# Kernel optimization log

Measured on AMD Instinct MI355X. Metric: run time of the kernel, lower is better.

## Reference

```python
import jax, jax.numpy as jnp
import numpy as np
import math

B, T, C, H, DFF = 4, 2048, 1024, 16, 4096
HD = C // H
EPS = 1e-5


def _layernorm(x, g, b):
    mu = jnp.mean(x, axis=-1, keepdims=True)
    var = jnp.var(x, axis=-1, keepdims=True)
    return (x - mu) * jax.lax.rsqrt(var + EPS) * g + b


def _new_gelu(x):
    # 0.5*x*(1+tanh(sqrt(2/pi)*(x+0.044715*x^3)))
    c = math.sqrt(2.0 / math.pi)
    return 0.5 * x * (1.0 + jnp.tanh(c * (x + 0.044715 * x ** 3)))


def setup_inputs() -> dict:
    key = jax.random.key(0)
    ks = jax.random.split(key, 12)
    s = lambda fan_in: 1.0 / math.sqrt(fan_in)
    return {
        "x": jax.random.normal(ks[0], (B, T, C), jnp.float32),
        "ln1_g": jnp.ones((C,), jnp.float32),
        "ln1_b": jnp.zeros((C,), jnp.float32),
        "w_qkv": jax.random.normal(ks[1], (C, 3 * C), jnp.float32) * s(C),
        "b_qkv": jnp.zeros((3 * C,), jnp.float32),
        "w_o": jax.random.normal(ks[2], (C, C), jnp.float32) * s(C),
        "b_o": jnp.zeros((C,), jnp.float32),
        "ln2_g": jnp.ones((C,), jnp.float32),
        "ln2_b": jnp.zeros((C,), jnp.float32),
        "w_fc": jax.random.normal(ks[3], (C, DFF), jnp.float32) * s(C),
        "b_fc": jnp.zeros((DFF,), jnp.float32),
        "w_proj": jax.random.normal(ks[4], (DFF, C), jnp.float32) * s(DFF),
        "b_proj": jnp.zeros((C,), jnp.float32),
    }


def reference(x, ln1_g, ln1_b, w_qkv, b_qkv, w_o, b_o, ln2_g, ln2_b, w_fc, b_fc, w_proj, b_proj):
    # --- attention sub-block ---
    h = _layernorm(x, ln1_g, ln1_b)
    qkv = h @ w_qkv + b_qkv                                  # (B,T,3C)
    q, k, v = jnp.split(qkv, 3, axis=-1)
    q = q.reshape(B, T, H, HD).transpose(0, 2, 1, 3)          # (B,H,T,hd)
    k = k.reshape(B, T, H, HD).transpose(0, 2, 1, 3)
    v = v.reshape(B, T, H, HD).transpose(0, 2, 1, 3)
    scores = jnp.einsum("bhqd,bhkd->bhqk", q, k) / math.sqrt(HD)
    causal = jnp.tril(jnp.ones((T, T), jnp.bool_))            # (T,T)
    scores = jnp.where(causal[None, None], scores, -jnp.inf)
    probs = jax.nn.softmax(scores, axis=-1)
    attn = jnp.einsum("bhqk,bhkd->bhqd", probs, v)
    attn = attn.transpose(0, 2, 1, 3).reshape(B, T, C)
    x = x + attn @ w_o + b_o
    # --- MLP sub-block ---
    h2 = _layernorm(x, ln2_g, ln2_b)
    x = x + _new_gelu(h2 @ w_fc + b_fc) @ w_proj + b_proj
    return x
```

## Files before the change

kernel.cpp:

```cpp
#include <hip/hip_runtime.h>
#include <hip/hip_bf16.h>

using bf16 = __hip_bfloat16;
typedef __attribute__((ext_vector_type(8))) short bf16x8;
typedef __attribute__((ext_vector_type(4))) float f32x4;
typedef __attribute__((ext_vector_type(16))) float f32x16;

#define LOG2E 1.4426950408889634f

__device__ inline short f2b(float f) {
  __hip_bfloat16 h = __float2bfloat16(f);
  return *reinterpret_cast<short*>(&h);
}
__device__ inline float b2f(short s) {
  unsigned int u = ((unsigned int)(unsigned short)s) << 16;
  float f;
  __builtin_memcpy(&f, &u, 4);
  return f;
}
__device__ inline unsigned pk2(float a, float b) {
  return (unsigned)(unsigned short)f2b(a) |
         ((unsigned)(unsigned short)f2b(b) << 16);
}

__global__ __launch_bounds__(256) void transpose_cast_kernel(
    const float* __restrict__ in, bf16* __restrict__ out, int K, int N) {
  __shared__ float tile[32][33];
  int tx = threadIdx.x & 31;
  int ty = threadIdx.x >> 5;
  int n0 = blockIdx.x * 32, k0 = blockIdx.y * 32;
#pragma unroll
  for (int i = 0; i < 4; i++)
    tile[ty + i * 8][tx] = in[(size_t)(k0 + ty + i * 8) * N + n0 + tx];
  __syncthreads();
#pragma unroll
  for (int i = 0; i < 4; i++)
    out[(size_t)(n0 + ty + i * 8) * K + k0 + tx] =
        __float2bfloat16(tile[tx][ty + i * 8]);
}

__global__ __launch_bounds__(256) void transpose_v_kernel(
    const bf16* __restrict__ qkv, bf16* __restrict__ vt) {
  __shared__ short tile[64][66];
  const int bh = blockIdx.y;
  const int b = bh >> 4, h = bh & 15;
  const int t0 = blockIdx.x * 64;
  const int tid = threadIdx.x;
  const int r = tid >> 3, c8 = (tid & 7) * 8;
#pragma unroll
  for (int p = 0; p < 2; p++) {
    int t = r + p * 32;
    bf16x8 v = *(const bf16x8*)&qkv[(size_t)(b * 2048 + t0 + t) * 3072 + 2048 +
                                    h * 64 + c8];
#pragma unroll
    for (int i = 0; i < 8; i++) tile[t][c8 + i] = v[i];
  }
  __syncthreads();
#pragma unroll
  for (int p = 0; p < 2; p++) {
    int d = r + p * 32;
    int tt = c8;
    bf16x8 o;
#pragma unroll
    for (int i = 0; i < 8; i++) o[i] = tile[tt + i][d];
    *(bf16x8*)&vt[(size_t)(bh * 64 + d) * 2048 + t0 + tt] = o;
  }
}

__global__ __launch_bounds__(256) void ln_kernel(
    const float* __restrict__ x, const float* __restrict__ g,
    const float* __restrict__ b, bf16* __restrict__ out) {
  int row = blockIdx.x;
  const float4 v = ((const float4*)(x + (size_t)row * 1024))[threadIdx.x];
  float s = v.x + v.y + v.z + v.w;
  float ss = v.x * v.x + v.y * v.y + v.z * v.z + v.w * v.w;
#pragma unroll
  for (int off = 1; off < 64; off <<= 1) {
    s += __shfl_xor(s, off);
    ss += __shfl_xor(ss, off);
  }
  __shared__ float red[2][4];
  int w = threadIdx.x >> 6, lane = threadIdx.x & 63;
  if (lane == 0) { red[0][w] = s; red[1][w] = ss; }
  __syncthreads();
  s = red[0][0] + red[0][1] + red[0][2] + red[0][3];
  ss = red[1][0] + red[1][1] + red[1][2] + red[1][3];
  float mu = s * (1.0f / 1024.0f);
  float var = ss * (1.0f / 1024.0f) - mu * mu;
  float rstd = rsqrtf(var + 1e-5f);
  const float4 gv = ((const float4*)g)[threadIdx.x];
  const float4 bv = ((const float4*)b)[threadIdx.x];
  short4 o4;
  o4.x = f2b((v.x - mu) * rstd * gv.x + bv.x);
  o4.y = f2b((v.y - mu) * rstd * gv.y + bv.y);
  o4.z = f2b((v.z - mu) * rstd * gv.z + bv.z);
  o4.w = f2b((v.w - mu) * rstd * gv.w + bv.w);
  ((short4*)out)[(size_t)row * 256 + threadIdx.x] = o4;
}

template <int EPI>
__global__ __launch_bounds__(256) void gemm_bt_kernel(
    const bf16* __restrict__ A, const bf16* __restrict__ Bt,
    const float* __restrict__ bias, const float* __restrict__ res,
    void* __restrict__ out, int M, int N, int K) {
  __shared__ short As[128 * 32];
  __shared__ short Bs[128 * 32];
  const int tid = threadIdx.x;
  const int w = tid >> 6, lane = tid & 63;
  const int wr = w >> 1, wc = w & 1;
  const int brow = blockIdx.y, bcol = blockIdx.x;

  f32x4 acc[4][4] = {};

  const int nk = K >> 5;
  for (int kt = 0; kt < nk; kt++) {
    __syncthreads();
#pragma unroll
    for (int j = 0; j < 2; j++) {
      int c = (j * 4 + w) * 64 + lane;
      int row = c >> 2, k8 = (c & 3) * 8;
      const bf16* ga = A + (size_t)(brow * 128 + row) * K + kt * 32 + k8;
      __builtin_amdgcn_global_load_lds(
          (const __attribute__((address_space(1))) unsigned int*)ga,
          (__attribute__((address_space(3))) unsigned int*)(As + (j * 4 + w) * 512),
          16, 0, 0);
      const bf16* gb = Bt + (size_t)(bcol * 128 + row) * K + kt * 32 + k8;
      __builtin_amdgcn_global_load_lds(
          (const __attribute__((address_space(1))) unsigned int*)gb,
          (__attribute__((address_space(3))) unsigned int*)(Bs + (j * 4 + w) * 512),
          16, 0, 0);
    }
    __syncthreads();
    bf16x8 af[4], bfr[4];
#pragma unroll
    for (int m = 0; m < 4; m++)
      af[m] = *(const bf16x8*)&As[(wr * 64 + m * 16 + (lane & 15)) * 32 +
                                  (lane >> 4) * 8];
#pragma unroll
    for (int n = 0; n < 4; n++)
      bfr[n] = *(const bf16x8*)&Bs[(wc * 64 + n * 16 + (lane & 15)) * 32 +
                                   (lane >> 4) * 8];
#pragma unroll
    for (int m = 0; m < 4; m++)
#pragma unroll
      for (int n = 0; n < 4; n++)
        acc[m][n] = __builtin_amdgcn_mfma_f32_16x16x32_bf16(af[m], bfr[n],
                                                            acc[m][n], 0, 0, 0);
  }

#pragma unroll
  for (int m = 0; m < 4; m++)
#pragma unroll
    for (int n = 0; n < 4; n++) {
      int gr0 = brow * 128 + wr * 64 + m * 16 + (lane >> 4) * 4;
      int gc = bcol * 128 + wc * 64 + n * 16 + (lane & 15);
      float bia = bias[gc];
#pragma unroll
      for (int j = 0; j < 4; j++) {
        float v = acc[m][n][j] + bia;
        size_t idx = (size_t)(gr0 + j) * N + gc;
        if constexpr (EPI == 0) {
          ((bf16*)out)[idx] = __float2bfloat16(v);
        } else if constexpr (EPI == 1) {
          ((float*)out)[idx] = v + res[idx];
        } else {
          float u = 0.7978845608028654f * (v + 0.044715f * v * v * v);
          float t = exp2f(u * (2.0f * LOG2E));
          float th = 1.0f - 2.0f / (t + 1.0f);
          ((bf16*)out)[idx] = __float2bfloat16(0.5f * v * (1.0f + th));
        }
      }
    }
}

__global__ __launch_bounds__(256) void attn_kernel(
    const bf16* __restrict__ qkv, const bf16* __restrict__ vt,
    bf16* __restrict__ attn) {
  const int bh = blockIdx.x;
  const int qt = blockIdx.y;
  const int b = bh >> 4, h = bh & 15;
  const int tid = threadIdx.x, w = tid >> 6, lane = tid & 63;
  const int col = lane & 31;
  const int hi = lane >> 5;

  __shared__ short Kl[64 * 64];
  __shared__ short Vl[64 * 64];

  const int qbase = qt * 128 + w * 32;
  const int qglob = qbase + col;
  const size_t qrow = (size_t)(b * 2048 + qglob);

  bf16x8 qf[4];
#pragma unroll
  for (int dks = 0; dks < 4; dks++) {
    bf16x8 raw =
        *(const bf16x8*)&qkv[qrow * 3072 + h * 64 + dks * 16 + hi * 8];
#pragma unroll
    for (int i = 0; i < 8; i++) qf[dks][i] = f2b(b2f(raw[i]) * 0.125f);
  }

  f32x16 ot[2] = {};
  float m = -1e30f, l = 0.0f;

  const int ktend = qt * 2 + 1;
  for (int kt = 0; kt <= ktend; kt++) {
    const int kv0 = kt * 64;
    __syncthreads();
#pragma unroll
    for (int j = 0; j < 2; j++) {
      int c = (j * 4 + w) * 64 + lane;
      int row = c >> 3;
      int sw8 = ((c & 7) ^ (row & 7)) * 8;
      const bf16* gk =
          qkv + (size_t)(b * 2048 + kv0 + row) * 3072 + 1024 + h * 64 + sw8;
      __builtin_amdgcn_global_load_lds(
          (const __attribute__((address_space(1))) unsigned int*)gk,
          (__attribute__((address_space(3))) unsigned int*)(Kl + (j * 4 + w) * 512),
          16, 0, 0);
      const bf16* gv = vt + (size_t)(bh * 64 + row) * 2048 + kv0 + sw8;
      __builtin_amdgcn_global_load_lds(
          (const __attribute__((address_space(1))) unsigned int*)gv,
          (__attribute__((address_space(3))) unsigned int*)(Vl + (j * 4 + w) * 512),
          16, 0, 0);
    }
    __syncthreads();

    if (kv0 <= qbase + 31) {
      f32x16 st[2] = {};
#pragma unroll
      for (int s = 0; s < 2; s++) {
        int kvrow = s * 32 + col;
        int swz = kvrow & 7;
#pragma unroll
        for (int dks = 0; dks < 4; dks++) {
          int ch = (dks * 2 + hi) ^ swz;
          bf16x8 kf = *(const bf16x8*)&Kl[kvrow * 64 + ch * 8];
          st[s] = __builtin_amdgcn_mfma_f32_32x32x16_bf16(kf, qf[dks], st[s],
                                                          0, 0, 0);
        }
      }
      if (kv0 + 63 > qbase) {
#pragma unroll
        for (int s = 0; s < 2; s++)
#pragma unroll
          for (int r = 0; r < 16; r++) {
            int kv = kv0 + s * 32 + (r & 3) + 8 * (r >> 2) + 4 * hi;
            if (kv > qglob) st[s][r] = -1e30f;
          }
      }
      float pmax = -1e30f;
#pragma unroll
      for (int s = 0; s < 2; s++)
#pragma unroll
        for (int r = 0; r < 16; r++) pmax = fmaxf(pmax, st[s][r]);
      pmax = fmaxf(pmax, __shfl_xor(pmax, 32));
      float mnew = fmaxf(m, pmax);
      float corr = exp2f((m - mnew) * LOG2E);
      m = mnew;
      float rs = 0.0f;
#pragma unroll
      for (int s = 0; s < 2; s++)
#pragma unroll
        for (int r = 0; r < 16; r++) {
          float pv = exp2f((st[s][r] - mnew) * LOG2E);
          st[s][r] = pv;
          rs += pv;
        }
      rs += __shfl_xor(rs, 32);
      l = l * corr + rs;
#pragma unroll
      for (int s = 0; s < 2; s++)
#pragma unroll
        for (int r = 0; r < 16; r++) ot[s][r] *= corr;

#pragma unroll
      for (int sub = 0; sub < 2; sub++) {
#pragma unroll
        for (int kl = 0; kl < 2; kl++) {
          unsigned A0 = pk2(st[sub][kl * 8 + 0], st[sub][kl * 8 + 1]);
          unsigned A1 = pk2(st[sub][kl * 8 + 2], st[sub][kl * 8 + 3]);
          unsigned B0 = pk2(st[sub][kl * 8 + 4], st[sub][kl * 8 + 5]);
          unsigned B1 = pk2(st[sub][kl * 8 + 6], st[sub][kl * 8 + 7]);
          unsigned sA0 = (unsigned)__shfl_xor((int)A0, 32);
          unsigned sA1 = (unsigned)__shfl_xor((int)A1, 32);
          unsigned sB0 = (unsigned)__shfl_xor((int)B0, 32);
          unsigned sB1 = (unsigned)__shfl_xor((int)B1, 32);
          union { unsigned u[4]; bf16x8 v; } pf;
          pf.u[0] = hi ? sB0 : A0;
          pf.u[1] = hi ? sB1 : A1;
          pf.u[2] = hi ? B0 : sA0;
          pf.u[3] = hi ? B1 : sA1;
          int ks = sub * 2 + kl;
#pragma unroll
          for (int ds = 0; ds < 2; ds++) {
            int drow = ds * 32 + col;
            int ch = (ks * 2 + hi) ^ (drow & 7);
            bf16x8 vf = *(const bf16x8*)&Vl[drow * 64 + ch * 8];
            ot[ds] = __builtin_amdgcn_mfma_f32_32x32x16_bf16(vf, pf.v, ot[ds],
                                                             0, 0, 0);
          }
        }
      }
    }
  }

  float rl = 1.0f / l;
#pragma unroll
  for (int ds = 0; ds < 2; ds++)
#pragma unroll
    for (int j = 0; j < 4; j++) {
      ushort4 o4;
      o4.x = (unsigned short)f2b(ot[ds][4 * j + 0] * rl);
      o4.y = (unsigned short)f2b(ot[ds][4 * j + 1] * rl);
      o4.z = (unsigned short)f2b(ot[ds][4 * j + 2] * rl);
      o4.w = (unsigned short)f2b(ot[ds][4 * j + 3] * rl);
      *(ushort4*)&attn[qrow * 1024 + h * 64 + 32 * ds + 8 * j + 4 * hi] = o4;
    }
}

extern "C" void kernel_launch(void* const* d_in, const int* in_sizes, int n_in,
                              void* d_out, int out_size, void* d_ws,
                              size_t ws_size, hipStream_t stream) {
  (void)in_sizes; (void)n_in; (void)out_size; (void)ws_size;
  const float* x      = (const float*)d_in[0];
  const float* ln1_g  = (const float*)d_in[1];
  const float* ln1_b  = (const float*)d_in[2];
  const float* w_qkv  = (const float*)d_in[3];
  const float* b_qkv  = (const float*)d_in[4];
  const float* w_o    = (const float*)d_in[5];
  const float* b_o    = (const float*)d_in[6];
  const float* ln2_g  = (const float*)d_in[7];
  const float* ln2_b  = (const float*)d_in[8];
  const float* w_fc   = (const float*)d_in[9];
  const float* b_fc   = (const float*)d_in[10];
  const float* w_proj = (const float*)d_in[11];
  const float* b_proj = (const float*)d_in[12];
  float* out = (float*)d_out;

  char* ws = (char*)d_ws;
  bf16* wt_qkv  = (bf16*)(ws + 0);
  bf16* wt_o    = (bf16*)(ws + 6291456);
  bf16* wt_fc   = (bf16*)(ws + 8388608);
  bf16* wt_proj = (bf16*)(ws + 16777216);
  float* x1     = (float*)(ws + 25165824);
  bf16* vtb     = (bf16*)(ws + 25165824);
  bf16* slotA   = (bf16*)(ws + 58720256);
  bf16* qkvb    = (bf16*)(ws + 75497472);
  bf16* gbuf    = (bf16*)(ws + 75497472);

  dim3 blk(256);
  transpose_cast_kernel<<<dim3(3072 / 32, 1024 / 32), blk, 0, stream>>>(
      w_qkv, wt_qkv, 1024, 3072);
  transpose_cast_kernel<<<dim3(1024 / 32, 1024 / 32), blk, 0, stream>>>(
      w_o, wt_o, 1024, 1024);
  transpose_cast_kernel<<<dim3(4096 / 32, 1024 / 32), blk, 0, stream>>>(
      w_fc, wt_fc, 1024, 4096);
  transpose_cast_kernel<<<dim3(1024 / 32, 4096 / 32), blk, 0, stream>>>(
      w_proj, wt_proj, 4096, 1024);

  ln_kernel<<<8192, blk, 0, stream>>>(x, ln1_g, ln1_b, slotA);
  gemm_bt_kernel<0><<<dim3(3072 / 128, 8192 / 128), blk, 0, stream>>>(
      slotA, wt_qkv, b_qkv, nullptr, qkvb, 8192, 3072, 1024);
  transpose_v_kernel<<<dim3(32, 64), blk, 0, stream>>>(qkvb, vtb);
  attn_kernel<<<dim3(64, 16), blk, 0, stream>>>(qkvb, vtb, slotA);
  gemm_bt_kernel<1><<<dim3(1024 / 128, 8192 / 128), blk, 0, stream>>>(
      slotA, wt_o, b_o, x, x1, 8192, 1024, 1024);
  ln_kernel<<<8192, blk, 0, stream>>>(x1, ln2_g, ln2_b, slotA);
  gemm_bt_kernel<2><<<dim3(4096 / 128, 8192 / 128), blk, 0, stream>>>(
      slotA, wt_fc, b_fc, nullptr, gbuf, 8192, 4096, 1024);
  gemm_bt_kernel<1><<<dim3(1024 / 128, 8192 / 128), blk, 0, stream>>>(
      gbuf, wt_proj, b_proj, x1, out, 8192, 1024, 4096);
}
```

Measured before the change: 471.3 us.

## Replace GEMM with 8-wave 128x256 double-buffered pipelined MFMA kernel

Measured after the change: 480.5 us. Within noise of the previous version (+2.0%).

```diff
diff --git a/kernel.cpp b/kernel.cpp
--- a/kernel.cpp
+++ b/kernel.cpp
@@ -98,54 +98,125 @@
   ((short4*)out)[(size_t)row * 256 + threadIdx.x] = o4;
 }
 
+template <int MLO, int NLO>
+__device__ inline void quad_mfma(f32x4 (&acc)[4][4], bf16x8 (&af)[2][2],
+                                 bf16x8 (&bf)[2][2]) {
+  __builtin_amdgcn_s_barrier();
+  asm volatile("s_waitcnt lgkmcnt(0)" ::: "memory");
+  __builtin_amdgcn_sched_barrier(0);
+  __builtin_amdgcn_s_setprio(1);
+#pragma unroll
+  for (int mm = 0; mm < 2; mm++)
+#pragma unroll
+    for (int nn = 0; nn < 2; nn++)
+#pragma unroll
+      for (int ks = 0; ks < 2; ks++)
+        acc[MLO + mm][NLO + nn] = __builtin_amdgcn_mfma_f32_16x16x32_bf16(
+            af[mm][ks], bf[nn][ks], acc[MLO + mm][NLO + nn], 0, 0, 0);
+  __builtin_amdgcn_s_setprio(0);
+  __builtin_amdgcn_s_barrier();
+}
+
 template <int EPI>
-__global__ __launch_bounds__(256) void gemm_bt_kernel(
+__global__ __launch_bounds__(512, 1) void gemm_bt8_kernel(
     const bf16* __restrict__ A, const bf16* __restrict__ Bt,
     const float* __restrict__ bias, const float* __restrict__ res,
     void* __restrict__ out, int M, int N, int K) {
-  __shared__ short As[128 * 32];
-  __shared__ short Bs[128 * 32];
+  __shared__ short As[2][128 * 64];
+  __shared__ short Bs[2][256 * 64];
   const int tid = threadIdx.x;
-  const int w = tid >> 6, lane = tid & 63;
-  const int wr = w >> 1, wc = w & 1;
-  const int brow = blockIdx.y, bcol = blockIdx.x;
+  const int lane = tid & 63, wid = tid >> 6;
+  const int wr = wid >> 2, wc = wid & 3;
+
+  const int nwg = gridDim.x;
+  const int gy = M >> 7;
+  const int flat = blockIdx.x;
+  const int sw = (flat & 7) * (nwg >> 3) + (flat >> 3);
+  const int bcol = sw / gy, brow = sw % gy;
+
+  const int nk = K >> 6;
+
+  auto stA = [&](int kt, int buf) {
+#pragma unroll
+    for (int r = 0; r < 2; r++) {
+      const int row = tid >> 3;
+      const int chs = (tid & 7) ^ (row & 7);
+      const bf16* src =
+          A + (size_t)(brow * 128 + r * 64 + row) * K + kt * 64 + chs * 8;
+      __builtin_amdgcn_global_load_lds(
+          (const __attribute__((address_space(1))) unsigned int*)src,
+          (__attribute__((address_space(3))) unsigned int*)
+              &As[buf][(r * 64 + wid * 8) * 64],
+          16, 0, 0);
+    }
+  };
+  auto stB = [&](int kt, int buf, int r0) {
+#pragma unroll
+    for (int rr = 0; rr < 2; rr++) {
+      const int r = r0 + rr;
+      const int row = tid >> 3;
+      const int chs = (tid & 7) ^ (row & 7);
+      const bf16* src =
+          Bt + (size_t)(bcol * 256 + r * 64 + row) * K + kt * 64 + chs * 8;
+      __builtin_amdgcn_global_load_lds(
+          (const __attribute__((address_space(1))) unsigned int*)src,
+          (__attribute__((address_space(3))) unsigned int*)
+              &Bs[buf][(r * 64 + wid * 8) * 64],
+          16, 0, 0);
+    }
+  };
 
   f32x4 acc[4][4] = {};
-
-  const int nk = K >> 5;
-  for (int kt = 0; kt < nk; kt++) {
-    __syncthreads();
-#pragma unroll
-    for (int j = 0; j < 2; j++) {
-      int c = (j * 4 + w) * 64 + lane;
-      int row = c >> 2, k8 = (c & 3) * 8;
-      const bf16* ga = A + (size_t)(brow * 128 + row) * K + kt * 32 + k8;
-      __builtin_amdgcn_global_load_lds(
-          (const __attribute__((address_space(1))) unsigned int*)ga,
-          (__attribute__((address_space(3))) unsigned int*)(As + (j * 4 + w) * 512),
-          16, 0, 0);
-      const bf16* gb = Bt + (size_t)(bcol * 128 + row) * K + kt * 32 + k8;
-      __builtin_amdgcn_global_load_lds(
-          (const __attribute__((address_space(1))) unsigned int*)gb,
-          (__attribute__((address_space(3))) unsigned int*)(Bs + (j * 4 + w) * 512),
-          16, 0, 0);
-    }
-    __syncthreads();
-    bf16x8 af[4], bfr[4];
-#pragma unroll
-    for (int m = 0; m < 4; m++)
-      af[m] = *(const bf16x8*)&As[(wr * 64 + m * 16 + (lane & 15)) * 32 +
-                                  (lane >> 4) * 8];
-#pragma unroll
-    for (int n = 0; n < 4; n++)
-      bfr[n] = *(const bf16x8*)&Bs[(wc * 64 + n * 16 + (lane & 15)) * 32 +
-                                   (lane >> 4) * 8];
-#pragma unroll
-    for (int m = 0; m < 4; m++)
-#pragma unroll
-      for (int n = 0; n < 4; n++)
-        acc[m][n] = __builtin_amdgcn_mfma_f32_16x16x32_bf16(af[m], bfr[n],
-                                                            acc[m][n], 0, 0, 0);
+  bf16x8 af[2][2], bf0[2][2], bf1[2][2];
+  int cur = 0;
+
+  auto rdA = [&](int mh) {
+#pragma unroll
+    for (int mm = 0; mm < 2; mm++)
+#pragma unroll
+      for (int ks = 0; ks < 2; ks++) {
+        const int row = wr * 64 + (mh * 2 + mm) * 16 + (lane & 15);
+        const int ch = (ks * 4 + (lane >> 4)) ^ (row & 7);
+        af[mm][ks] = *(const bf16x8*)&As[cur][row * 64 + ch * 8];
+      }
+  };
+  auto rdB = [&](bf16x8(&bf)[2][2], int nh) {
+#pragma unroll
+    for (int nn = 0; nn < 2; nn++)
+#pragma unroll
+      for (int ks = 0; ks < 2; ks++) {
+        const int row = wc * 64 + (nh * 2 + nn) * 16 + (lane & 15);
+        const int ch = (ks * 4 + (lane >> 4)) ^ (row & 7);
+        bf[nn][ks] = *(const bf16x8*)&Bs[cur][row * 64 + ch * 8];
+      }
+  };
+
+  stA(0, 0);
+  stB(0, 0, 0);
+  stB(0, 0, 2);
+  stA(1, 1);
+  asm volatile("s_waitcnt vmcnt(2)" ::: "memory");
+  __builtin_amdgcn_s_barrier();
+
+  for (int t = 0; t < nk; t++) {
+    cur = t & 1;
+    const int nxt = cur ^ 1;
+    rdA(0);
+    rdB(bf0, 0);
+    if (t + 1 < nk) stB(t + 1, nxt, 0);
+    quad_mfma<0, 0>(acc, af, bf0);
+    rdB(bf1, 1);
+    if (t + 1 < nk) stB(t + 1, nxt, 2);
+    quad_mfma<0, 2>(acc, af, bf1);
+    rdA(1);
+    quad_mfma<2, 2>(acc, af, bf1);
+    if (t + 2 < nk) {
+      stA(t + 2, cur);
+      asm volatile("s_waitcnt vmcnt(2)" ::: "memory");
+    } else if (t + 1 < nk) {
+      asm volatile("s_waitcnt vmcnt(0)" ::: "memory");
+    }
+    quad_mfma<2, 0>(acc, af, bf0);
   }
 
 #pragma unroll
@@ -153,7 +224,7 @@
 #pragma unroll
     for (int n = 0; n < 4; n++) {
       int gr0 = brow * 128 + wr * 64 + m * 16 + (lane >> 4) * 4;
-      int gc = bcol * 128 + wc * 64 + n * 16 + (lane & 15);
+      int gc = bcol * 256 + wc * 64 + n * 16 + (lane & 15);
       float bia = bias[gc];
 #pragma unroll
       for (int j = 0; j < 4; j++) {
@@ -165,8 +236,8 @@
           ((float*)out)[idx] = v + res[idx];
         } else {
           float u = 0.7978845608028654f * (v + 0.044715f * v * v * v);
-          float t = exp2f(u * (2.0f * LOG2E));
-          float th = 1.0f - 2.0f / (t + 1.0f);
+          float t2 = exp2f(u * (2.0f * LOG2E));
+          float th = 1.0f - 2.0f / (t2 + 1.0f);
           ((bf16*)out)[idx] = __float2bfloat16(0.5f * v * (1.0f + th));
         }
       }
@@ -359,15 +430,15 @@
       w_proj, wt_proj, 4096, 1024);
 
   ln_kernel<<<8192, blk, 0, stream>>>(x, ln1_g, ln1_b, slotA);
-  gemm_bt_kernel<0><<<dim3(3072 / 128, 8192 / 128), blk, 0, stream>>>(
+  gemm_bt8_kernel<0><<<dim3(768), dim3(512), 0, stream>>>(
       slotA, wt_qkv, b_qkv, nullptr, qkvb, 8192, 3072, 1024);
   transpose_v_kernel<<<dim3(32, 64), blk, 0, stream>>>(qkvb, vtb);
   attn_kernel<<<dim3(64, 16), blk, 0, stream>>>(qkvb, vtb, slotA);
-  gemm_bt_kernel<1><<<dim3(1024 / 128, 8192 / 128), blk, 0, stream>>>(
+  gemm_bt8_kernel<1><<<dim3(256), dim3(512), 0, stream>>>(
       slotA, wt_o, b_o, x, x1, 8192, 1024, 1024);
   ln_kernel<<<8192, blk, 0, stream>>>(x1, ln2_g, ln2_b, slotA);
-  gemm_bt_kernel<2><<<dim3(4096 / 128, 8192 / 128), blk, 0, stream>>>(
+  gemm_bt8_kernel<2><<<dim3(1024), dim3(512), 0, stream>>>(
       slotA, wt_fc, b_fc, nullptr, gbuf, 8192, 4096, 1024);
-  gemm_bt_kernel<1><<<dim3(1024 / 128, 8192 / 128), blk, 0, stream>>>(
+  gemm_bt8_kernel<1><<<dim3(256), dim3(512), 0, stream>>>(
       gbuf, wt_proj, b_proj, x1, out, 8192, 1024, 4096);
 }
```
